# Kernel optimization log

Measured on AMD Instinct MI355X. Metric: run time of the kernel, lower is better.

Reference implementation:

```python
import jax, jax.numpy as jnp
import numpy as np

B, S, DIM, N, D = 1, 3072, 2048, 16, 128
EPS = 1e-06


def rms_norm(x, w, eps=EPS):
    # x: [B, S, C]; normalize over last dim (matches npu_rms_norm)
    var = jnp.mean(jnp.square(x), axis=-1, keepdims=True)
    return x * jax.lax.rsqrt(var + eps) * w


def rope_interleave(x, cos, sin):
    # x: [B, S, N, D]; cos/sin: [B, S, 1, D] with pairwise-repeated values.
    # interleave mode: (x0, x1) -> (x0*c - x1*s, x1*c + x0*s) for adjacent pairs.
    xe = x[..., 0::2]
    xo = x[..., 1::2]
    rot = jnp.stack([-xo, xe], axis=-1).reshape(x.shape)
    return (x * cos + rot * sin).astype(jnp.float32)  # rope_apply casts to float


def setup_inputs() -> dict:
    key = jax.random.key(0)
    ks = jax.random.split(key, 16)
    sd = 1.0 / np.sqrt(DIM)
    inp = {
        'x': jax.random.normal(ks[0], (B, S, DIM), jnp.float32),
        'Wq': jax.random.normal(ks[1], (DIM, DIM), jnp.float32) * sd,
        'bq': jax.random.normal(ks[2], (DIM,), jnp.float32) * 0.01,
        'Wk': jax.random.normal(ks[3], (DIM, DIM), jnp.float32) * sd,
        'bk': jax.random.normal(ks[4], (DIM,), jnp.float32) * 0.01,
        'Wv': jax.random.normal(ks[5], (DIM, DIM), jnp.float32) * sd,
        'bv': jax.random.normal(ks[6], (DIM,), jnp.float32) * 0.01,
        'Wo': jax.random.normal(ks[7], (DIM, DIM), jnp.float32) * sd,
        'bo': jax.random.normal(ks[8], (DIM,), jnp.float32) * 0.01,
        'norm_q_w': jnp.ones((DIM,), jnp.float32),
        'norm_k_w': jnp.ones((DIM,), jnp.float32),
    }
    # per-sample 3D rope folded into precomputed interleaved cos/sin tables
    pos = jnp.arange(S, dtype=jnp.float32)
    inv = 1.0 / (10000.0 ** (jnp.arange(D // 2, dtype=jnp.float32) / (D // 2)))
    ang = pos[:, None] * inv[None, :]                    # [S, D/2]
    cos = jnp.repeat(jnp.cos(ang), 2, axis=-1)           # [S, D] pairwise repeated
    sin = jnp.repeat(jnp.sin(ang), 2, axis=-1)
    inp['rope_cos'] = jnp.broadcast_to(cos[None, :, None, :], (B, S, 1, D))
    inp['rope_sin'] = jnp.broadcast_to(sin[None, :, None, :], (B, S, 1, D))
    inp['seq_lens'] = jax.random.randint(ks[9], (B,), S // 2, S + 1).astype(jnp.int32)
    inp['grid_sizes'] = jnp.broadcast_to(jnp.array([[12, 16, 16]], jnp.int32), (B, 3))
    return inp


def reference(x, Wq, bq, Wk, bk, Wv, bv, Wo, bo, norm_q_w, norm_k_w,
              rope_cos, rope_sin, seq_lens, grid_sizes):
    b, s, _ = x.shape
    # fused QKV projection + RMSNorm on q/k
    q = rms_norm(x @ Wq.T + bq, norm_q_w).reshape(b, s, N, D)
    k = rms_norm(x @ Wk.T + bk, norm_k_w).reshape(b, s, N, D)
    v = (x @ Wv.T + bv).reshape(b, s, N, D)
    # per-sample interleaved RoPE (outputs float32, as in rope_apply)
    q = rope_interleave(q, rope_cos, rope_sin)
    k = rope_interleave(k, rope_cos, rope_sin)
    # full attention with key-length masking (window_size = (-1, -1))
    scale = 1.0 / np.sqrt(D)
    scores = jnp.einsum('bqnd,bknd->bnqk', q, k) * scale    # [B, N, S, S]
    kmask = jnp.arange(s)[None, :] < seq_lens[:, None]       # [B, S]
    scores = jnp.where(kmask[:, None, None, :], scores, jnp.float32(-1e30))
    probs = jax.nn.softmax(scores, axis=-1)
    out = jnp.einsum('bnqk,bknd->bqnd', probs, v.astype(jnp.float32))
    out = out.reshape(b, s, N * D)
    return out @ Wo.T + bo
```

## Files before the change

### kernel.cpp

```cpp
#include <hip/hip_runtime.h>

typedef __attribute__((ext_vector_type(8))) short short8;
typedef __attribute__((ext_vector_type(4))) float f32x4;

#define SQ 3072
#define DM 2048
#define NHEAD 16
#define HDIM 128

__device__ __forceinline__ unsigned short f2bf(float f) {
  union { float f; unsigned int u; } un; un.f = f;
  unsigned int r = un.u + 0x7fffu + ((un.u >> 16) & 1u);
  return (unsigned short)(r >> 16);
}

__device__ __forceinline__ void gload_lds16(const void* g, void* l) {
  __builtin_amdgcn_global_load_lds(
      (const __attribute__((address_space(1))) void*)g,
      (__attribute__((address_space(3))) void*)l, 16, 0, 0);
}

__global__ __launch_bounds__(256) void cvt_all(
    const float* __restrict__ x, const float* __restrict__ wq, const float* __restrict__ wk,
    const float* __restrict__ wv, const float* __restrict__ wo,
    unsigned short* __restrict__ xb, unsigned short* __restrict__ wqkvb,
    unsigned short* __restrict__ wob)
{
  int b = blockIdx.x;
  const float* src; unsigned short* dst; int idx;
  if (b < 3072) { src = x; dst = xb; idx = b; }
  else {
    int r = b - 3072; int w = r >> 11; idx = r & 2047;
    src = (w == 0) ? wq : (w == 1) ? wk : (w == 2) ? wv : wo;
    dst = (w < 3) ? wqkvb + (size_t)w * DM * DM : wob;
  }
  int i = (idx * 256 + threadIdx.x) * 8;
  float4 a = *(const float4*)(src + i);
  float4 c = *(const float4*)(src + i + 4);
  short8 r;
  r[0] = (short)f2bf(a.x); r[1] = (short)f2bf(a.y);
  r[2] = (short)f2bf(a.z); r[3] = (short)f2bf(a.w);
  r[4] = (short)f2bf(c.x); r[5] = (short)f2bf(c.y);
  r[6] = (short)f2bf(c.z); r[7] = (short)f2bf(c.w);
  *(short8*)(dst + i) = r;
}

__global__ __launch_bounds__(512, 2) void gemm_nt_bias(
    const unsigned short* __restrict__ A, const unsigned short* __restrict__ B,
    const float* __restrict__ b0, const float* __restrict__ b1, const float* __restrict__ b2,
    float* __restrict__ C, int M, int N, int K, int nbm)
{
  __shared__ __align__(16) unsigned short lds[3 * 12288];
  const int tid = threadIdx.x;
  const int w = tid >> 6, l = tid & 63;
  const int wm = w >> 2, wn = w & 3;
  const int lr = l & 15, lg = l >> 4;

  const int nwg = gridDim.x;
  const int swz = (blockIdx.x & 7) * (nwg >> 3) + (blockIdx.x >> 3);
  const int m0 = (swz % nbm) * 128, n0 = (swz / nbm) * 256;

  const int srow = tid >> 2;
  const int scol = ((tid & 3) ^ ((tid >> 3) & 3)) * 8;
  const unsigned short* aS  = A + (size_t)(m0 + srow) * K + scol;
  const unsigned short* bS0 = B + (size_t)(n0 + srow) * K + scol;
  const unsigned short* bS1 = B + (size_t)(n0 + 128 + srow) * K + scol;
  const int ldst = w * 512;

  auto stage = [&](int t, int b) {
    unsigned short* base = &lds[b * 12288];
    const size_t tc = (size_t)t * 32;
    gload_lds16(aS + tc, base + ldst);
    gload_lds16(bS0 + tc, base + 4096 + ldst);
    gload_lds16(bS1 + tc, base + 8192 + ldst);
  };

  const int sx = ((lr >> 1) & 3);
  const int aoff = (wm * 64 + lr) * 32 + ((lg ^ sx) * 8);
  const int boff = 4096 + (wn * 64 + lr) * 32 + ((lg ^ sx) * 8);

  f32x4 acc[4][4] = {};
  const int nt = K >> 5;

  stage(0, 0); stage(1, 1);
  asm volatile("s_waitcnt vmcnt(3)" ::: "memory");
  __builtin_amdgcn_s_barrier();

  for (int t = 0; t < nt; ++t) {
    const unsigned short* buf = &lds[(t % 3) * 12288];
    if (t + 2 < nt) stage(t + 2, (t + 2) % 3);
    short8 af[4], bfr[4];
    #pragma unroll
    for (int m = 0; m < 4; ++m) af[m] = *(const short8*)&buf[aoff + m * 512];
    #pragma unroll
    for (int n = 0; n < 4; ++n) bfr[n] = *(const short8*)&buf[boff + n * 512];
    __builtin_amdgcn_s_setprio(1);
    #pragma unroll
    for (int m = 0; m < 4; ++m) {
      #pragma unroll
      for (int n = 0; n < 4; ++n)
        acc[m][n] = __builtin_amdgcn_mfma_f32_16x16x32_bf16(af[m], bfr[n], acc[m][n], 0, 0, 0);
    }
    __builtin_amdgcn_s_setprio(0);
    if (t + 2 < nt) {
      asm volatile("s_waitcnt vmcnt(3)" ::: "memory");
      __builtin_amdgcn_s_barrier();
    } else if (t + 2 == nt) {
      asm volatile("s_waitcnt vmcnt(0)" ::: "memory");
      __builtin_amdgcn_s_barrier();
    }
  }

  const float* bp = (n0 < DM) ? b0 : ((n0 < 2 * DM) ? b1 : b2);
  #pragma unroll
  for (int n = 0; n < 4; ++n) {
    int col = n0 + wn * 64 + n * 16 + lr;
    float bv = bp[col & (DM - 1)];
    #pragma unroll
    for (int m = 0; m < 4; ++m) {
      int row = m0 + wm * 64 + m * 16 + lg * 4;
      #pragma unroll
      for (int j = 0; j < 4; ++j)
        C[(size_t)(row + j) * N + col] = acc[m][n][j] + bv;
    }
  }
}

__global__ __launch_bounds__(256) void normrope(
    const float* __restrict__ qkv, const float* __restrict__ nqw, const float* __restrict__ nkw,
    const float* __restrict__ cosb, const float* __restrict__ sinb,
    unsigned short* __restrict__ Qb, unsigned short* __restrict__ Kb)
{
  const int s = blockIdx.x, z = blockIdx.y;
  const float* row = qkv + ((size_t)s * 3 + z) * DM;
  const float* gw = z ? nkw : nqw;
  unsigned short* ob = z ? Kb : Qb;
  const int t = threadIdx.x;
  float v[8];
  {
    float4 a = *(const float4*)(row + t * 8);
    float4 b = *(const float4*)(row + t * 8 + 4);
    v[0] = a.x; v[1] = a.y; v[2] = a.z; v[3] = a.w;
    v[4] = b.x; v[5] = b.y; v[6] = b.z; v[7] = b.w;
  }
  float ss = 0.f;
  #pragma unroll
  for (int i = 0; i < 8; ++i) ss += v[i] * v[i];
  #pragma unroll
  for (int off = 1; off < 64; off <<= 1) ss += __shfl_xor(ss, off);
  __shared__ float red[4];
  const int wave = t >> 6, lane = t & 63;
  if (lane == 0) red[wave] = ss;
  __syncthreads();
  float tot = red[0] + red[1] + red[2] + red[3];
  float rsc = rsqrtf(tot * (1.0f / 2048.0f) + 1e-6f);
  const float qs = z ? 1.0f : 0.12751879522087045f;
  const int col = t * 8, d = col & 127, h = col >> 7;
  const float* cb = cosb + (size_t)s * HDIM + d;
  const float* sb = sinb + (size_t)s * HDIM + d;
  float y[8];
  #pragma unroll
  for (int i = 0; i < 8; ++i) y[i] = v[i] * rsc * gw[col + i];
  short8 r;
  #pragma unroll
  for (int p = 0; p < 4; ++p) {
    float e = y[2 * p], o = y[2 * p + 1];
    float c0 = cb[2 * p], s0 = sb[2 * p];
    float c1 = cb[2 * p + 1], s1 = sb[2 * p + 1];
    r[2 * p]     = (short)f2bf((e * c0 - o * s0) * qs);
    r[2 * p + 1] = (short)f2bf((o * c1 + e * s1) * qs);
  }
  *(short8*)(ob + ((size_t)h * SQ + s) * HDIM + d) = r;
}

__global__ __launch_bounds__(256) void vtrans(const float* __restrict__ V, int ldv,
                                              unsigned short* __restrict__ Vt)
{
  __shared__ float tile[64][65];
  const int db = blockIdx.x * 64, sb = blockIdx.y * 64, h = blockIdx.z;
  const int t = threadIdx.x;
  const int rr = t >> 2, c0 = (t & 3) * 16;
  const float* src = V + (size_t)(sb + rr) * ldv + h * HDIM + db + c0;
  #pragma unroll
  for (int i = 0; i < 4; ++i) {
    float4 a = *(const float4*)(src + i * 4);
    tile[rr][c0 + i * 4 + 0] = a.x; tile[rr][c0 + i * 4 + 1] = a.y;
    tile[rr][c0 + i * 4 + 2] = a.z; tile[rr][c0 + i * 4 + 3] = a.w;
  }
  __syncthreads();
  const int dr = t >> 2, s0 = (t & 3) * 16;
  short8 r0, r1;
  #pragma unroll
  for (int i = 0; i < 8; ++i) r0[i] = (short)f2bf(tile[s0 + i][dr]);
  #pragma unroll
  for (int i = 0; i < 8; ++i) r1[i] = (short)f2bf(tile[s0 + 8 + i][dr]);
  unsigned short* dst = Vt + ((size_t)h * HDIM + db + dr) * SQ + sb + s0;
  *(short8*)(dst) = r0;
  *(short8*)(dst + 8) = r1;
}

__global__ __launch_bounds__(256) void attn(
    const unsigned short* __restrict__ Qb, const unsigned short* __restrict__ Kb,
    const unsigned short* __restrict__ Vt, const int* __restrict__ seq_lens,
    unsigned short* __restrict__ aout)
{
  __shared__ __align__(16) unsigned short Ks[64 * 136];
  __shared__ __align__(16) unsigned short Vs[128 * 72];
  __shared__ __align__(16) unsigned short Ps[4][16 * 72];
  const int tid = threadIdx.x, wave = tid >> 6, lane = tid & 63;
  const int h = blockIdx.y, q0 = blockIdx.x * 64;
  const int lr = lane & 15, lg = lane >> 4;
  const int seq_len = seq_lens[0];

  short8 qf[4];
  {
    const unsigned short* qrow = Qb + ((size_t)h * SQ + q0 + wave * 16 + lr) * HDIM;
    #pragma unroll
    for (int kk = 0; kk < 4; ++kk)
      qf[kk] = *(const short8*)(qrow + kk * 32 + lg * 8);
  }
  f32x4 o[8] = {};
  float lsum[4] = {0.f, 0.f, 0.f, 0.f};

  for (int kt = 0; kt < seq_len; kt += 64) {
    #pragma unroll
    for (int c = 0; c < 4; ++c) {
      int lin = c * 256 + tid;
      int krow = lin >> 4, kc = (lin & 15) * 8;
      short8 tv = *(const short8*)(Kb + ((size_t)h * SQ + kt + krow) * HDIM + kc);
      *(short8*)&Ks[krow * 136 + kc] = tv;
    }
    #pragma unroll
    for (int c = 0; c < 4; ++c) {
      int lin = c * 256 + tid;
      int vrow = lin >> 3, vc = (lin & 7) * 8;
      short8 tv = *(const short8*)(Vt + ((size_t)h * HDIM + vrow) * SQ + kt + vc);
      *(short8*)&Vs[vrow * 72 + vc] = tv;
    }
    __syncthreads();

    f32x4 sf[4] = {};
    #pragma unroll
    for (int kk = 0; kk < 4; ++kk) {
      #pragma unroll
      for (int n = 0; n < 4; ++n) {
        short8 kf = *(const short8*)&Ks[(n * 16 + lr) * 136 + kk * 32 + lg * 8];
        sf[n] = __builtin_amdgcn_mfma_f32_16x16x32_bf16(qf[kk], kf, sf[n], 0, 0, 0);
      }
    }
    if (kt + 64 > seq_len) {
      #pragma unroll
      for (int n = 0; n < 4; ++n) {
        if (kt + n * 16 + lr >= seq_len) {
          #pragma unroll
          for (int j = 0; j < 4; ++j) sf[n][j] = -3.0e38f;
        }
      }
    }
    unsigned short* Pw = &Ps[wave][0];
    #pragma unroll
    for (int n = 0; n < 4; ++n) {
      #pragma unroll
      for (int j = 0; j < 4; ++j) {
        float p = exp2f(sf[n][j]);
        lsum[j] += p;
        Pw[(lg * 4 + j) * 72 + n * 16 + lr] = f2bf(p);
      }
    }
    #pragma unroll
    for (int kk = 0; kk < 2; ++kk) {
      short8 pa = *(const short8*)&Pw[lr * 72 + kk * 32 + lg * 8];
      #pragma unroll
      for (int dn = 0; dn < 8; ++dn) {
        short8 vb = *(const short8*)&Vs[(dn * 16 + lr) * 72 + kk * 32 + lg * 8];
        o[dn] = __builtin_amdgcn_mfma_f32_16x16x32_bf16(pa, vb, o[dn], 0, 0, 0);
      }
    }
    __syncthreads();
  }
  #pragma unroll
  for (int off = 1; off < 16; off <<= 1) {
    #pragma unroll
    for (int j = 0; j < 4; ++j) lsum[j] += __shfl_xor(lsum[j], off);
  }
  float rcp[4];
  #pragma unroll
  for (int j = 0; j < 4; ++j) rcp[j] = 1.0f / lsum[j];
  #pragma unroll
  for (int dn = 0; dn < 8; ++dn) {
    int col = h * HDIM + dn * 16 + lr;
    #pragma unroll
    for (int j = 0; j < 4; ++j) {
      int row = q0 + wave * 16 + lg * 4 + j;
      aout[(size_t)row * DM + col] = f2bf(o[dn][j] * rcp[j]);
    }
  }
}

extern "C" void kernel_launch(void* const* d_in, const int* in_sizes, int n_in,
                              void* d_out, int out_size, void* d_ws, size_t ws_size,
                              hipStream_t stream) {
  const float* x   = (const float*)d_in[0];
  const float* Wq  = (const float*)d_in[1];
  const float* bq  = (const float*)d_in[2];
  const float* Wk  = (const float*)d_in[3];
  const float* bk  = (const float*)d_in[4];
  const float* Wv  = (const float*)d_in[5];
  const float* bv  = (const float*)d_in[6];
  const float* Wo  = (const float*)d_in[7];
  const float* bo  = (const float*)d_in[8];
  const float* nqw = (const float*)d_in[9];
  const float* nkw = (const float*)d_in[10];
  const float* rc  = (const float*)d_in[11];
  const float* rs  = (const float*)d_in[12];
  const int* seql  = (const int*)d_in[13];
  float* out = (float*)d_out;

  unsigned short* xb   = (unsigned short*)d_ws;
  unsigned short* Wqkv = xb   + (size_t)SQ * DM;
  unsigned short* Wob  = Wqkv + (size_t)3 * DM * DM;
  float* qkv           = (float*)(Wob + (size_t)DM * DM);
  unsigned short* Qb   = (unsigned short*)(qkv + (size_t)3 * SQ * DM);
  unsigned short* Kb   = Qb + (size_t)SQ * DM;
  unsigned short* Vt   = Kb + (size_t)SQ * DM;
  unsigned short* aob  = Vt + (size_t)SQ * DM;

  cvt_all<<<3072 + 4 * 2048, 256, 0, stream>>>(x, Wq, Wk, Wv, Wo, xb, Wqkv, Wob);

  gemm_nt_bias<<<(SQ / 128) * (3 * DM / 256), 512, 0, stream>>>(
      xb, Wqkv, bq, bk, bv, qkv, SQ, 3 * DM, DM, SQ / 128);

  normrope<<<dim3(SQ, 2), 256, 0, stream>>>(qkv, nqw, nkw, rc, rs, Qb, Kb);
  vtrans<<<dim3(2, SQ / 64, NHEAD), 256, 0, stream>>>(qkv + 2 * DM, 3 * DM, Vt);

  attn<<<dim3(SQ / 64, NHEAD), 256, 0, stream>>>(Qb, Kb, Vt, seql, aob);

  gemm_nt_bias<<<(SQ / 128) * (DM / 256), 512, 0, stream>>>(
      aob, Wob, bo, bo, bo, out, SQ, DM, DM, SQ / 128);
}
```

Measured before the change: 405.3 us.

## Prefetch next K/V tile into registers and tune attention inner loop

The attention kernel now loads the next 64-key K and V tile into registers while the current tile is being computed, so global memory latency overlaps with MFMA work. It also raises wave priority around the MFMA blocks, switches to the hardware exp2 intrinsic and the HIP bf16 conversion, and pads the per-wave P buffer stride to 76 to reduce LDS bank conflicts. The prefetch costs extra VGPRs, which may lower occupancy.

```diff
diff --git a/kernel.cpp b/kernel.cpp
--- a/kernel.cpp
+++ b/kernel.cpp
@@ -1,4 +1,5 @@
 #include <hip/hip_runtime.h>
+#include <hip/hip_bf16.h>
 
 typedef __attribute__((ext_vector_type(8))) short short8;
 typedef __attribute__((ext_vector_type(4))) float f32x4;
@@ -12,6 +13,11 @@
   union { float f; unsigned int u; } un; un.f = f;
   unsigned int r = un.u + 0x7fffu + ((un.u >> 16) & 1u);
   return (unsigned short)(r >> 16);
+}
+
+__device__ __forceinline__ unsigned short f2bf_hw(float f) {
+  __hip_bfloat16 h = __float2bfloat16(f);
+  return *reinterpret_cast<unsigned short*>(&h);
 }
 
 __device__ __forceinline__ void gload_lds16(const void* g, void* l) {
@@ -199,6 +205,7 @@
   *(short8*)(dst + 8) = r1;
 }
 
+#define PST 76
 __global__ __launch_bounds__(256) void attn(
     const unsigned short* __restrict__ Qb, const unsigned short* __restrict__ Kb,
     const unsigned short* __restrict__ Vt, const int* __restrict__ seq_lens,
@@ -206,7 +213,7 @@
 {
   __shared__ __align__(16) unsigned short Ks[64 * 136];
   __shared__ __align__(16) unsigned short Vs[128 * 72];
-  __shared__ __align__(16) unsigned short Ps[4][16 * 72];
+  __shared__ __align__(16) unsigned short Ps[4][16 * PST];
   const int tid = threadIdx.x, wave = tid >> 6, lane = tid & 63;
   const int h = blockIdx.y, q0 = blockIdx.x * 64;
   const int lr = lane & 15, lg = lane >> 4;
@@ -222,24 +229,35 @@
   f32x4 o[8] = {};
   float lsum[4] = {0.f, 0.f, 0.f, 0.f};
 
+  const unsigned short* kSrc = Kb + ((size_t)h * SQ + (tid >> 4)) * HDIM + (tid & 15) * 8;
+  const unsigned short* vSrc = Vt + ((size_t)h * HDIM + (tid >> 3)) * SQ + (tid & 7) * 8;
+  unsigned short* kDst = &Ks[(tid >> 4) * 136 + (tid & 15) * 8];
+  unsigned short* vDst = &Vs[(tid >> 3) * 72 + (tid & 7) * 8];
+
+  short8 kreg[4], vreg[4];
+  #pragma unroll
+  for (int c = 0; c < 4; ++c) {
+    kreg[c] = *(const short8*)(kSrc + (size_t)c * 16 * HDIM);
+    vreg[c] = *(const short8*)(vSrc + (size_t)c * 32 * SQ);
+  }
+
   for (int kt = 0; kt < seq_len; kt += 64) {
     #pragma unroll
     for (int c = 0; c < 4; ++c) {
-      int lin = c * 256 + tid;
-      int krow = lin >> 4, kc = (lin & 15) * 8;
-      short8 tv = *(const short8*)(Kb + ((size_t)h * SQ + kt + krow) * HDIM + kc);
-      *(short8*)&Ks[krow * 136 + kc] = tv;
-    }
-    #pragma unroll
-    for (int c = 0; c < 4; ++c) {
-      int lin = c * 256 + tid;
-      int vrow = lin >> 3, vc = (lin & 7) * 8;
-      short8 tv = *(const short8*)(Vt + ((size_t)h * HDIM + vrow) * SQ + kt + vc);
-      *(short8*)&Vs[vrow * 72 + vc] = tv;
+      *(short8*)(kDst + c * 16 * 136) = kreg[c];
+      *(short8*)(vDst + c * 32 * 72) = vreg[c];
+    }
+    if (kt + 64 < seq_len) {
+      #pragma unroll
+      for (int c = 0; c < 4; ++c) {
+        kreg[c] = *(const short8*)(kSrc + ((size_t)(kt + 64) + c * 16) * HDIM);
+        vreg[c] = *(const short8*)(vSrc + (size_t)(kt + 64) + (size_t)c * 32 * SQ);
+      }
     }
     __syncthreads();
 
     f32x4 sf[4] = {};
+    __builtin_amdgcn_s_setprio(1);
     #pragma unroll
     for (int kk = 0; kk < 4; ++kk) {
       #pragma unroll
@@ -248,6 +266,7 @@
         sf[n] = __builtin_amdgcn_mfma_f32_16x16x32_bf16(qf[kk], kf, sf[n], 0, 0, 0);
       }
     }
+    __builtin_amdgcn_s_setprio(0);
     if (kt + 64 > seq_len) {
       #pragma unroll
       for (int n = 0; n < 4; ++n) {
@@ -262,19 +281,21 @@
     for (int n = 0; n < 4; ++n) {
       #pragma unroll
       for (int j = 0; j < 4; ++j) {
-        float p = exp2f(sf[n][j]);
+        float p = __builtin_amdgcn_exp2f(sf[n][j]);
         lsum[j] += p;
-        Pw[(lg * 4 + j) * 72 + n * 16 + lr] = f2bf(p);
+        Pw[(lg * 4 + j) * PST + n * 16 + lr] = f2bf_hw(p);
       }
     }
     #pragma unroll
     for (int kk = 0; kk < 2; ++kk) {
-      short8 pa = *(const short8*)&Pw[lr * 72 + kk * 32 + lg * 8];
+      short8 pa = *(const short8*)&Pw[lr * PST + kk * 32 + lg * 8];
+      __builtin_amdgcn_s_setprio(1);
       #pragma unroll
       for (int dn = 0; dn < 8; ++dn) {
         short8 vb = *(const short8*)&Vs[(dn * 16 + lr) * 72 + kk * 32 + lg * 8];
         o[dn] = __builtin_amdgcn_mfma_f32_16x16x32_bf16(pa, vb, o[dn], 0, 0, 0);
       }
+      __builtin_amdgcn_s_setprio(0);
     }
     __syncthreads();
   }
@@ -292,7 +313,7 @@
     #pragma unroll
     for (int j = 0; j < 4; ++j) {
       int row = q0 + wave * 16 + lg * 4 + j;
-      aout[(size_t)row * DM + col] = f2bf(o[dn][j] * rcp[j]);
+      aout[(size_t)row * DM + col] = f2bf_hw(o[dn][j] * rcp[j]);
     }
   }
 }
```

Result: slower. 425.0 us (+4.8%).
